# Optimization experiments

Hardware: AMD Instinct MI355X
Metric: run time of the kernel (lower is better)

Reference implementation:

```python
import jax, jax.numpy as jnp
import numpy as np

B, S, D = 1, 2048, 4096
H, KV = 32, 8
HD = D // H  # 128
NEG = -1e9


def _rope(t, cos, sin):
    # t: [B,S,h,HD]; cos/sin: [S,HD//2] -> broadcast [1,S,1,HD//2]
    tr = t[..., 0::2]
    ti = t[..., 1::2]
    c = cos[None, :, None, :]
    s = sin[None, :, None, :]
    out_r = tr * c - ti * s
    out_i = tr * s + ti * c
    # interleave back: (..., HD//2, 2) -> (..., HD)
    return jnp.stack([out_r, out_i], axis=-1).reshape(t.shape)


def setup_inputs() -> dict:
    key = jax.random.key(0)
    ks = jax.random.split(key, 5)
    w_scale = 0.02
    x = jax.random.normal(ks[0], (B, S, D), dtype=jnp.float32)
    wq = jax.random.normal(ks[1], (H * HD, D), dtype=jnp.float32) * w_scale
    wk = jax.random.normal(ks[2], (KV * HD, D), dtype=jnp.float32) * w_scale
    wv = jax.random.normal(ks[3], (KV * HD, D), dtype=jnp.float32) * w_scale
    wo = jax.random.normal(ks[4], (D, H * HD), dtype=jnp.float32) * w_scale
    # RoPE tables (theta = 10000)
    inv_freq = 1.0 / (10000.0 ** (np.arange(0, HD, 2, dtype=np.float32) / HD))
    angles = np.arange(S, dtype=np.float32)[:, None] * inv_freq[None, :]  # [S, HD//2]
    freqs_cos = jnp.asarray(np.cos(angles))
    freqs_sin = jnp.asarray(np.sin(angles))
    # causal additive mask [1,1,S,S]
    causal = jnp.tril(jnp.ones((S, S), dtype=bool))
    mask = jnp.where(causal, 0.0, NEG).astype(jnp.float32)[None, None]
    return {"x": x, "wq": wq, "wk": wk, "wv": wv, "wo": wo,
            "freqs_cos": freqs_cos, "freqs_sin": freqs_sin, "mask": mask}


def reference(x, wq, wk, wv, wo, freqs_cos, freqs_sin, mask):
    b, s, d = x.shape
    q = (x @ wq.T).reshape(b, s, H, HD)
    k = (x @ wk.T).reshape(b, s, KV, HD)
    v = (x @ wv.T).reshape(b, s, KV, HD)
    q = _rope(q, freqs_cos, freqs_sin)
    k = _rope(k, freqs_cos, freqs_sin)
    rep = H // KV
    k = jnp.repeat(k, rep, axis=2)  # [b,s,H,HD]
    v = jnp.repeat(v, rep, axis=2)
    scores = jnp.einsum('bshd,bthd->bhst', q, k) / jnp.sqrt(jnp.float32(HD))
    scores = scores + mask
    attn = jax.nn.softmax(scores, axis=-1)
    out = jnp.einsum('bhst,bthd->bshd', attn, v).reshape(b, s, H * HD)
    return out @ wo.T
```

## Files before the change

kernel.cpp:

```cpp
#include <hip/hip_runtime.h>
#include <hip/hip_bf16.h>
#include <math.h>

#define SEQ 2048
#define DIM 4096
#define NH 32
#define NKV 8
#define HD 128
#define KVD 1024
#define SCALE 0.08838834764831845f
#define NEGBIG -1000000000.0f

typedef __bf16 bf16;
typedef __attribute__((ext_vector_type(2))) __bf16 bf16x2;
typedef __attribute__((ext_vector_type(4))) __bf16 bf16x4;
typedef __attribute__((ext_vector_type(8))) __bf16 bf16x8;
typedef __attribute__((ext_vector_type(4))) float f32x4;

__device__ __forceinline__ void async_g2l16(const bf16* g, bf16* l) {
  __builtin_amdgcn_global_load_lds(
      (const __attribute__((address_space(1))) void*)g,
      (__attribute__((address_space(3))) void*)l,
      16, 0, 0);
}

#define SEG_X  2097152
#define SEG_WQ 4194304
#define SEG_WK 1048576
#define C0 SEG_X
#define C1 (C0 + SEG_WQ)
#define C2 (C1 + SEG_WK)
#define C3 (C2 + SEG_WK)
#define C4 (C3 + SEG_WQ)

__global__ void cast_all_kernel(const float* __restrict__ x,
                                const float* __restrict__ wq,
                                const float* __restrict__ wk,
                                const float* __restrict__ wv,
                                const float* __restrict__ wo,
                                bf16* __restrict__ xb, bf16* __restrict__ wqb,
                                bf16* __restrict__ wkb, bf16* __restrict__ wvb,
                                bf16* __restrict__ wob) {
  int i = blockIdx.x * 256 + threadIdx.x;
  const float* src; bf16* dst; int j;
  if (i < C0)      { src = x;  dst = xb;  j = i; }
  else if (i < C1) { src = wq; dst = wqb; j = i - C0; }
  else if (i < C2) { src = wk; dst = wkb; j = i - C1; }
  else if (i < C3) { src = wv; dst = wvb; j = i - C2; }
  else             { src = wo; dst = wob; j = i - C3; }
  float4 v = ((const float4*)src)[j];
  bf16x4 o;
  o[0] = (bf16)v.x; o[1] = (bf16)v.y; o[2] = (bf16)v.z; o[3] = (bf16)v.w;
  ((bf16x4*)dst)[j] = o;
}

__device__ __forceinline__ void gemm_core(
    const bf16* __restrict__ A, int lda,
    const bf16* __restrict__ B, int ldb,
    int K, int mBase, f32x4 acc[4][4])
{
  __shared__ __align__(16) bf16 As[128 * 32];
  __shared__ __align__(16) bf16 Bs[128 * 32];

  const int tid  = threadIdx.x;
  const int lane = tid & 63;
  const int w    = tid >> 6;
  const int l15  = lane & 15;
  const int quad = lane >> 4;
  const int wr   = (w >> 1) * 64;
  const int wc   = (w & 1) * 64;

  const int srow = lane >> 2;
  const int kswz = ((lane & 3) ^ ((srow >> 1) & 3)) * 8;
  const bf16* gA0 = A + (size_t)(mBase + w * 16 + srow) * lda + kswz;
  const bf16* gA1 = gA0 + (size_t)64 * lda;
  const bf16* gB0 = B + (size_t)(w * 16 + srow) * ldb + kswz;
  const bf16* gB1 = gB0 + (size_t)64 * ldb;
  bf16* lA0 = As + w * 512;
  bf16* lA1 = As + (w + 4) * 512;
  bf16* lB0 = Bs + w * 512;
  bf16* lB1 = Bs + (w + 4) * 512;

  const f32x4 vzero = {0.f, 0.f, 0.f, 0.f};
#pragma unroll
  for (int mi = 0; mi < 4; ++mi)
#pragma unroll
    for (int ni = 0; ni < 4; ++ni) acc[mi][ni] = vzero;

  const int rsw = ((l15 >> 1) & 3);

  for (int k0 = 0; k0 < K; k0 += 32) {
    __syncthreads();
    async_g2l16(gA0 + k0, lA0);
    async_g2l16(gA1 + k0, lA1);
    async_g2l16(gB0 + k0, lB0);
    async_g2l16(gB1 + k0, lB1);
    __syncthreads();

    bf16x8 a[4], b[4];
#pragma unroll
    for (int mi = 0; mi < 4; ++mi)
      a[mi] = *(const bf16x8*)(As + (wr + mi * 16 + l15) * 32 +
                               ((quad ^ rsw) * 8));
#pragma unroll
    for (int ni = 0; ni < 4; ++ni)
      b[ni] = *(const bf16x8*)(Bs + (wc + ni * 16 + l15) * 32 +
                               ((quad ^ rsw) * 8));
#pragma unroll
    for (int mi = 0; mi < 4; ++mi)
#pragma unroll
      for (int ni = 0; ni < 4; ++ni)
        acc[mi][ni] = __builtin_amdgcn_mfma_f32_16x16x32_bf16(
            a[mi], b[ni], acc[mi][ni], 0, 0, 0);
  }
}

__global__ __launch_bounds__(256, 2) void qkv_gemm_kernel(
    const bf16* __restrict__ xb, const bf16* __restrict__ wqb,
    const bf16* __restrict__ wkb, const bf16* __restrict__ wvb,
    const float* __restrict__ fc, const float* __restrict__ fs,
    bf16* __restrict__ Qb, bf16* __restrict__ Kb, bf16* __restrict__ Vt)
{
  const int nb = blockIdx.x;
  const int mBase = blockIdx.y * 128;
  const bf16* Bm;
  if (nb < 32)      Bm = wqb + (size_t)nb * 128 * DIM;
  else if (nb < 40) Bm = wkb + (size_t)(nb - 32) * 128 * DIM;
  else              Bm = wvb + (size_t)(nb - 40) * 128 * DIM;

  f32x4 acc[4][4];
  gemm_core(xb, DIM, Bm, DIM, DIM, mBase, acc);

  const int tid  = threadIdx.x;
  const int lane = tid & 63;
  const int w    = tid >> 6;
  const int l15  = lane & 15;
  const int quad = lane >> 4;
  const int wr   = (w >> 1) * 64;
  const int wc   = (w & 1) * 64;

  if (nb < 40) {
    const bool isQ = (nb < 32);
    bf16* dst = isQ ? (Qb + nb * HD) : (Kb + (nb - 32) * HD);
    const int ldd = isQ ? DIM : KVD;
    const float sc = isQ ? SCALE : 1.0f;
    const int odd = l15 & 1;
#pragma unroll
    for (int mi = 0; mi < 4; ++mi) {
#pragma unroll
      for (int ni = 0; ni < 4; ++ni) {
        int d = wc + ni * 16 + l15;
        int fidx = d >> 1;
#pragma unroll
        for (int r = 0; r < 4; ++r) {
          int s = mBase + wr + mi * 16 + quad * 4 + r;
          float v  = acc[mi][ni][r];
          float pv = __shfl_xor(v, 1, 64);
          float c  = fc[s * 64 + fidx];
          float sn = fs[s * 64 + fidx];
          float o  = odd ? (pv * sn + v * c) : (v * c - pv * sn);
          dst[(size_t)s * ldd + d] = (bf16)(o * sc);
        }
      }
    }
  } else {
    const int t = nb - 40;
#pragma unroll
    for (int mi = 0; mi < 4; ++mi) {
      int srow = mBase + wr + mi * 16 + quad * 4;
#pragma unroll
      for (int ni = 0; ni < 4; ++ni) {
        int d = wc + ni * 16 + l15;
        bf16x4 pv;
#pragma unroll
        for (int r = 0; r < 4; ++r) pv[r] = (bf16)acc[mi][ni][r];
        *(bf16x4*)(Vt + ((size_t)t * HD + d) * SEQ + srow) = pv;
      }
    }
  }
}

__global__ __launch_bounds__(256, 2) void out_gemm_kernel(
    const bf16* __restrict__ attnb, const bf16* __restrict__ wob,
    float* __restrict__ out)
{
  const int mBase = blockIdx.y * 128;
  f32x4 acc[4][4];
  gemm_core(attnb, DIM, wob + (size_t)blockIdx.x * 128 * DIM, DIM, DIM,
            mBase, acc);

  const int tid  = threadIdx.x;
  const int lane = tid & 63;
  const int w    = tid >> 6;
  const int l15  = lane & 15;
  const int quad = lane >> 4;
  const int wr   = (w >> 1) * 64;
  const int wc   = (w & 1) * 64;
#pragma unroll
  for (int mi = 0; mi < 4; ++mi) {
    int row = mBase + wr + mi * 16 + quad * 4;
#pragma unroll
    for (int ni = 0; ni < 4; ++ni) {
      int col = blockIdx.x * 128 + wc + ni * 16 + l15;
#pragma unroll
      for (int r = 0; r < 4; ++r)
        out[(size_t)(row + r) * DIM + col] = acc[mi][ni][r];
    }
  }
}

__global__ __launch_bounds__(256, 2) void attn_kernel(
    const bf16* __restrict__ Qb, const bf16* __restrict__ Kb,
    const bf16* __restrict__ Vt, bf16* __restrict__ attnb)
{
  __shared__ __align__(16) bf16 Ks[64 * 128];
  __shared__ __align__(16) bf16 Vs[128 * 64];
  __shared__ __align__(16) bf16 Ps[128 * 64];

  const int b    = blockIdx.x;
  const int half = b >> 8;
  const int r8   = b & 255;
  const int h    = (half << 4) | (r8 >> 4);
  const int qt   = half ? (r8 & 15) : 15 - (r8 & 15);
  const int kvh  = h >> 2;
  const int qbase = qt * 128;

  const int tid  = threadIdx.x;
  const int lane = tid & 63;
  const int w    = tid >> 6;
  const int l15  = lane & 15;
  const int quad = lane >> 4;

  bf16x8 qfrag[2][4];
#pragma unroll
  for (int n = 0; n < 2; ++n) {
    int q = qbase + w * 32 + n * 16 + l15;
#pragma unroll
    for (int ks = 0; ks < 4; ++ks)
      qfrag[n][ks] = *(const bf16x8*)(Qb + (size_t)q * DIM + h * HD +
                                      ks * 32 + quad * 8);
  }

  const f32x4 vzero = {0.f, 0.f, 0.f, 0.f};
  f32x4 oacc[8][2];
#pragma unroll
  for (int dm = 0; dm < 8; ++dm)
#pragma unroll
    for (int n = 0; n < 2; ++n) oacc[dm][n] = vzero;
  float m_run[2] = {-1e30f, -1e30f};
  float l_run[2] = {0.f, 0.f};

  const int nkt = 2 * (qt + 1);
  for (int kt = 0; kt < nkt; ++kt) {
    const int kbase = kt * 64;

    __syncthreads();
#pragma unroll
    for (int t = 0; t < 4; ++t) {
      int kr0 = w * 16 + t * 4;
      int krow = kr0 + (lane >> 4);
      int kg = (lane & 15) ^ (krow & 7);
      async_g2l16(Kb + (size_t)(kbase + krow) * KVD + kvh * HD + kg * 8,
                  Ks + kr0 * 128);
      int vr0 = w * 32 + t * 8;
      int d = vr0 + (lane >> 3);
      int vg = (lane & 7) ^ (d & 7);
      async_g2l16(Vt + ((size_t)kvh * HD + d) * SEQ + kbase + vg * 8,
                  Vs + vr0 * 64);
    }
    __syncthreads();

    f32x4 sacc[4][2];
#pragma unroll
    for (int kg = 0; kg < 4; ++kg)
#pragma unroll
      for (int n = 0; n < 2; ++n) sacc[kg][n] = vzero;
#pragma unroll
    for (int kg = 0; kg < 4; ++kg) {
      bf16x8 kf[4];
#pragma unroll
      for (int ks = 0; ks < 4; ++ks) {
        int row = kg * 16 + l15;
        kf[ks] = *(const bf16x8*)(Ks + row * 128 +
                                  (((ks * 4 + quad) ^ (row & 7)) * 8));
      }
#pragma unroll
      for (int n = 0; n < 2; ++n)
#pragma unroll
        for (int ks = 0; ks < 4; ++ks)
          sacc[kg][n] = __builtin_amdgcn_mfma_f32_16x16x32_bf16(
              kf[ks], qfrag[n][ks], sacc[kg][n], 0, 0, 0);
    }

#pragma unroll
    for (int n = 0; n < 2; ++n) {
      const int qloc = w * 32 + n * 16 + l15;
      const int qglob = qbase + qloc;
      if (kbase + 63 > qbase + w * 32 + n * 16) {
#pragma unroll
        for (int kg = 0; kg < 4; ++kg)
#pragma unroll
          for (int r = 0; r < 4; ++r) {
            int key = kbase + kg * 16 + quad * 4 + r;
            if (key > qglob) sacc[kg][n][r] = NEGBIG;
          }
      }
      float mx = -1e30f;
#pragma unroll
      for (int kg = 0; kg < 4; ++kg)
#pragma unroll
        for (int r = 0; r < 4; ++r) mx = fmaxf(mx, sacc[kg][n][r]);
      mx = fmaxf(mx, __shfl_xor(mx, 16, 64));
      mx = fmaxf(mx, __shfl_xor(mx, 32, 64));
      float mnew = fmaxf(m_run[n], mx);
      float alpha = __expf(m_run[n] - mnew);
      m_run[n] = mnew;
      float rs = 0.f;
#pragma unroll
      for (int kg = 0; kg < 4; ++kg) {
        bf16x4 pk;
#pragma unroll
        for (int r = 0; r < 4; ++r) {
          float p = __expf(sacc[kg][n][r] - mnew);
          rs += p;
          pk[r] = (bf16)p;
        }
        int g16 = (kg * 2 + (quad >> 1)) ^ (qloc & 7);
        *(bf16x4*)(Ps + qloc * 64 + g16 * 8 + (quad & 1) * 4) = pk;
      }
      rs += __shfl_xor(rs, 16, 64);
      rs += __shfl_xor(rs, 32, 64);
      l_run[n] = alpha * l_run[n] + rs;
#pragma unroll
      for (int dm = 0; dm < 8; ++dm)
#pragma unroll
        for (int r = 0; r < 4; ++r) oacc[dm][n][r] *= alpha;
    }

    bf16x8 pf[2][2];
#pragma unroll
    for (int kk = 0; kk < 2; ++kk)
#pragma unroll
      for (int n = 0; n < 2; ++n) {
        int qloc = w * 32 + n * 16 + l15;
        pf[kk][n] = *(const bf16x8*)(Ps + qloc * 64 +
                                     (((kk * 4 + quad) ^ (qloc & 7)) * 8));
      }
#pragma unroll
    for (int dm = 0; dm < 8; ++dm) {
#pragma unroll
      for (int kk = 0; kk < 2; ++kk) {
        int d = dm * 16 + l15;
        bf16x8 vf = *(const bf16x8*)(Vs + d * 64 +
                                     (((kk * 4 + quad) ^ (d & 7)) * 8));
#pragma unroll
        for (int n = 0; n < 2; ++n)
          oacc[dm][n] = __builtin_amdgcn_mfma_f32_16x16x32_bf16(
              vf, pf[kk][n], oacc[dm][n], 0, 0, 0);
      }
    }
  }

#pragma unroll
  for (int n = 0; n < 2; ++n) {
    float inv = 1.0f / l_run[n];
    int q = qbase + w * 32 + n * 16 + l15;
#pragma unroll
    for (int dm = 0; dm < 8; ++dm) {
      bf16x4 ov;
#pragma unroll
      for (int r = 0; r < 4; ++r) ov[r] = (bf16)(oacc[dm][n][r] * inv);
      *(bf16x4*)(attnb + (size_t)q * DIM + h * HD + dm * 16 + quad * 4) = ov;
    }
  }
}

extern "C" void kernel_launch(void* const* d_in, const int* in_sizes, int n_in,
                              void* d_out, int out_size, void* d_ws, size_t ws_size,
                              hipStream_t stream) {
  const float* x  = (const float*)d_in[0];
  const float* wq = (const float*)d_in[1];
  const float* wk = (const float*)d_in[2];
  const float* wv = (const float*)d_in[3];
  const float* wo = (const float*)d_in[4];
  const float* fc = (const float*)d_in[5];
  const float* fs = (const float*)d_in[6];
  float* out = (float*)d_out;

  size_t off = 0;
  char* wsb = (char*)d_ws;
  auto take = [&](size_t bytes) -> void* {
    void* p = wsb + off;
    off += (bytes + 255) & ~(size_t)255;
    return p;
  };
  bf16*  xb    = (bf16*)take((size_t)SEQ * DIM * 2);
  bf16*  wqb   = (bf16*)take((size_t)DIM * DIM * 2);
  bf16*  wkb   = (bf16*)take((size_t)KVD * DIM * 2);
  bf16*  wvb   = (bf16*)take((size_t)KVD * DIM * 2);
  bf16*  wob   = (bf16*)take((size_t)DIM * DIM * 2);
  bf16*  Qb    = (bf16*)take((size_t)SEQ * DIM * 2);
  bf16*  Kb    = (bf16*)take((size_t)SEQ * KVD * 2);
  bf16*  Vt    = (bf16*)take((size_t)NKV * HD * SEQ * 2);
  bf16*  attnb = (bf16*)take((size_t)SEQ * DIM * 2);

  cast_all_kernel<<<C4 / 256, 256, 0, stream>>>(x, wq, wk, wv, wo,
                                                xb, wqb, wkb, wvb, wob);

  qkv_gemm_kernel<<<dim3(48, 16), 256, 0, stream>>>(xb, wqb, wkb, wvb,
                                                    fc, fs, Qb, Kb, Vt);

  attn_kernel<<<dim3(512), 256, 0, stream>>>(Qb, Kb, Vt, attnb);

  out_gemm_kernel<<<dim3(32, 16), 256, 0, stream>>>(attnb, wob, out);
}
```

Measured before the change: 482.4 us.

## Replace GEMMs with 256x256 double-buffered, ping-pong scheduled 8-wave kernel

Both projection GEMMs now use a 256x256 block tile with 512 threads, K-tiles of 64, double-buffered LDS and async global-to-LDS loads interleaved between MFMA quarter-steps, with barriers and setprio to alternate waves between memory and math. This targets the old 128x128, K=32 single-buffer loop, which synchronised twice per step and exposed load latency. In exchange it uses a large LDS footprint (128KB) and high register pressure, and launches fewer blocks (192 and 128 across a 256-CU part), which may leave CUs idle.

Result: slower. 511.7 us (+6.1%).

```diff
diff --git a/kernel.cpp b/kernel.cpp
--- a/kernel.cpp
+++ b/kernel.cpp
@@ -12,7 +12,6 @@
 #define NEGBIG -1000000000.0f
 
 typedef __bf16 bf16;
-typedef __attribute__((ext_vector_type(2))) __bf16 bf16x2;
 typedef __attribute__((ext_vector_type(4))) __bf16 bf16x4;
 typedef __attribute__((ext_vector_type(8))) __bf16 bf16x8;
 typedef __attribute__((ext_vector_type(4))) float f32x4;
@@ -54,159 +53,235 @@
   ((bf16x4*)dst)[j] = o;
 }
 
-__device__ __forceinline__ void gemm_core(
-    const bf16* __restrict__ A, int lda,
-    const bf16* __restrict__ B, int ldb,
-    int K, int mBase, f32x4 acc[4][4])
+#define BAR()       asm volatile("s_barrier" ::: "memory")
+#define FENCE4()    asm volatile("s_waitcnt vmcnt(4)" ::: "memory")
+#define FENCE_ALL() asm volatile("s_waitcnt vmcnt(0)" ::: "memory")
+
+#define MFMAQ(AH, BC, MO, NO)                                              \
+  _Pragma("unroll") for (int m2 = 0; m2 < 4; ++m2)                         \
+  _Pragma("unroll") for (int n2 = 0; n2 < 2; ++n2)                         \
+  _Pragma("unroll") for (int kk = 0; kk < 2; ++kk)                         \
+    acc[(MO) + m2][(NO) + n2] = __builtin_amdgcn_mfma_f32_16x16x32_bf16(   \
+        (AH)[m2][kk], (BC)[n2][kk], acc[(MO) + m2][(NO) + n2], 0, 0, 0);
+
+__device__ __forceinline__ void gemm256_core(
+    const bf16* __restrict__ Ag,
+    const bf16* __restrict__ Bg,
+    f32x4 acc[8][4])
 {
-  __shared__ __align__(16) bf16 As[128 * 32];
-  __shared__ __align__(16) bf16 Bs[128 * 32];
+  __shared__ __align__(16) bf16 As[2 * 256 * 64];
+  __shared__ __align__(16) bf16 Bs[2 * 256 * 64];
 
   const int tid  = threadIdx.x;
   const int lane = tid & 63;
   const int w    = tid >> 6;
   const int l15  = lane & 15;
   const int quad = lane >> 4;
-  const int wr   = (w >> 1) * 64;
-  const int wc   = (w & 1) * 64;
-
-  const int srow = lane >> 2;
-  const int kswz = ((lane & 3) ^ ((srow >> 1) & 3)) * 8;
-  const bf16* gA0 = A + (size_t)(mBase + w * 16 + srow) * lda + kswz;
-  const bf16* gA1 = gA0 + (size_t)64 * lda;
-  const bf16* gB0 = B + (size_t)(w * 16 + srow) * ldb + kswz;
-  const bf16* gB1 = gB0 + (size_t)64 * ldb;
-  bf16* lA0 = As + w * 512;
-  bf16* lA1 = As + (w + 4) * 512;
-  bf16* lB0 = Bs + w * 512;
-  bf16* lB1 = Bs + (w + 4) * 512;
-
-  const f32x4 vzero = {0.f, 0.f, 0.f, 0.f};
-#pragma unroll
-  for (int mi = 0; mi < 4; ++mi)
-#pragma unroll
-    for (int ni = 0; ni < 4; ++ni) acc[mi][ni] = vzero;
-
-  const int rsw = ((l15 >> 1) & 3);
-
-  for (int k0 = 0; k0 < K; k0 += 32) {
-    __syncthreads();
-    async_g2l16(gA0 + k0, lA0);
-    async_g2l16(gA1 + k0, lA1);
-    async_g2l16(gB0 + k0, lB0);
-    async_g2l16(gB1 + k0, lB1);
-    __syncthreads();
-
-    bf16x8 a[4], b[4];
-#pragma unroll
-    for (int mi = 0; mi < 4; ++mi)
-      a[mi] = *(const bf16x8*)(As + (wr + mi * 16 + l15) * 32 +
-                               ((quad ^ rsw) * 8));
-#pragma unroll
-    for (int ni = 0; ni < 4; ++ni)
-      b[ni] = *(const bf16x8*)(Bs + (wc + ni * 16 + l15) * 32 +
-                               ((quad ^ rsw) * 8));
-#pragma unroll
-    for (int mi = 0; mi < 4; ++mi)
-#pragma unroll
-      for (int ni = 0; ni < 4; ++ni)
-        acc[mi][ni] = __builtin_amdgcn_mfma_f32_16x16x32_bf16(
-            a[mi], b[ni], acc[mi][ni], 0, 0, 0);
+  const int wr2  = (w >> 2) * 128;
+  const int wc2  = (w & 3) * 64;
+
+  const int srow = w * 8 + (lane >> 3);
+  const int sg8  = ((lane & 7) ^ (lane >> 3)) * 8;
+  const bf16* gA = Ag + (size_t)srow * DIM + sg8;
+  const bf16* gB = Bg + (size_t)srow * DIM + sg8;
+  bf16* lA = As + w * 512;
+  bf16* lB = Bs + w * 512;
+
+  const int g0   = (quad ^ (l15 & 7)) * 8;
+  const int g1   = g0 ^ 32;
+  const int aOff = (wr2 + l15) * 64;
+  const int bOff = (wc2 + l15) * 64;
+
+#define STAGE_A(b, kt)                                                     \
+  { _Pragma("unroll") for (int hh = 0; hh < 2; ++hh)                       \
+    _Pragma("unroll") for (int j = 0; j < 2; ++j)                          \
+      async_g2l16(gA + (size_t)(hh * 128 + j * 64) * DIM + (kt) * 64,      \
+                  lA + (b) * 16384 + (hh * 128 + j * 64) * 64); }
+#define STAGE_B0(b, kt)                                                    \
+  { _Pragma("unroll") for (int j = 0; j < 2; ++j)                          \
+      async_g2l16(gB + (size_t)(j * 64) * DIM + (kt) * 64,                 \
+                  lB + (b) * 16384 + (j * 64) * 64); }
+#define STAGE_B1(b, kt)                                                    \
+  { _Pragma("unroll") for (int j = 0; j < 2; ++j)                          \
+      async_g2l16(gB + (size_t)(128 + j * 64) * DIM + (kt) * 64,           \
+                  lB + (b) * 16384 + (128 + j * 64) * 64); }
+
+#define LDA(b, rh, m2, gk) \
+  (*(const bf16x8*)(As + (b) * 16384 + aOff + (rh) * 4096 + (m2) * 1024 + (gk)))
+#define LDB(b, ch, n2, gk) \
+  (*(const bf16x8*)(Bs + (b) * 16384 + bOff + (ch) * 2048 + (n2) * 1024 + (gk)))
+
+  const f32x4 vz = {0.f, 0.f, 0.f, 0.f};
+#pragma unroll
+  for (int mi = 0; mi < 8; ++mi)
+#pragma unroll
+    for (int ni = 0; ni < 4; ++ni) acc[mi][ni] = vz;
+
+  STAGE_A(0, 0); STAGE_B0(0, 0); STAGE_B1(0, 0);
+  STAGE_B0(1, 1); STAGE_B1(1, 1);
+  FENCE4();
+  BAR();
+
+  for (int i = 0; i < 32; ++i) {
+    const int ktn0 = (2 * i + 2 > 63) ? 63 : 2 * i + 2;
+    const int ktn1 = (2 * i + 3 > 63) ? 63 : 2 * i + 3;
+    {
+      bf16x8 aH[4][2], bC0[2][2], bC1[2][2];
+#pragma unroll
+      for (int m2 = 0; m2 < 4; ++m2) { aH[m2][0] = LDA(0, 0, m2, g0); aH[m2][1] = LDA(0, 0, m2, g1); }
+#pragma unroll
+      for (int n2 = 0; n2 < 2; ++n2) { bC0[n2][0] = LDB(0, 0, n2, g0); bC0[n2][1] = LDB(0, 0, n2, g1); }
+      STAGE_A(1, 2 * i + 1);
+      BAR(); __builtin_amdgcn_s_setprio(1);
+      MFMAQ(aH, bC0, 0, 0);
+      __builtin_amdgcn_s_setprio(0); BAR();
+#pragma unroll
+      for (int n2 = 0; n2 < 2; ++n2) { bC1[n2][0] = LDB(0, 1, n2, g0); bC1[n2][1] = LDB(0, 1, n2, g1); }
+      BAR(); __builtin_amdgcn_s_setprio(1);
+      MFMAQ(aH, bC1, 0, 2);
+      __builtin_amdgcn_s_setprio(0); BAR();
+#pragma unroll
+      for (int m2 = 0; m2 < 4; ++m2) { aH[m2][0] = LDA(0, 1, m2, g0); aH[m2][1] = LDA(0, 1, m2, g1); }
+      STAGE_B0(0, ktn0);
+      BAR(); __builtin_amdgcn_s_setprio(1);
+      MFMAQ(aH, bC1, 4, 2);
+      __builtin_amdgcn_s_setprio(0); BAR();
+      STAGE_B1(0, ktn0);
+      FENCE4();
+      BAR(); __builtin_amdgcn_s_setprio(1);
+      MFMAQ(aH, bC0, 4, 0);
+      __builtin_amdgcn_s_setprio(0); BAR();
+    }
+    {
+      bf16x8 aH[4][2], bC0[2][2], bC1[2][2];
+#pragma unroll
+      for (int m2 = 0; m2 < 4; ++m2) { aH[m2][0] = LDA(1, 0, m2, g0); aH[m2][1] = LDA(1, 0, m2, g1); }
+#pragma unroll
+      for (int n2 = 0; n2 < 2; ++n2) { bC0[n2][0] = LDB(1, 0, n2, g0); bC0[n2][1] = LDB(1, 0, n2, g1); }
+      STAGE_A(0, ktn0);
+      BAR(); __builtin_amdgcn_s_setprio(1);
+      MFMAQ(aH, bC0, 0, 0);
+      __builtin_amdgcn_s_setprio(0); BAR();
+#pragma unroll
+      for (int n2 = 0; n2 < 2; ++n2) { bC1[n2][0] = LDB(1, 1, n2, g0); bC1[n2][1] = LDB(1, 1, n2, g1); }
+      BAR(); __builtin_amdgcn_s_setprio(1);
+      MFMAQ(aH, bC1, 0, 2);
+      __builtin_amdgcn_s_setprio(0); BAR();
+#pragma unroll
+      for (int m2 = 0; m2 < 4; ++m2) { aH[m2][0] = LDA(1, 1, m2, g0); aH[m2][1] = LDA(1, 1, m2, g1); }
+      STAGE_B0(1, ktn1);
+      BAR(); __builtin_amdgcn_s_setprio(1);
+      MFMAQ(aH, bC1, 4, 2);
+      __builtin_amdgcn_s_setprio(0); BAR();
+      STAGE_B1(1, ktn1);
+      FENCE4();
+      BAR(); __builtin_amdgcn_s_setprio(1);
+      MFMAQ(aH, bC0, 4, 0);
+      __builtin_amdgcn_s_setprio(0); BAR();
+    }
   }
-}
-
-__global__ __launch_bounds__(256, 2) void qkv_gemm_kernel(
+  FENCE_ALL();
+}
+
+__global__ __launch_bounds__(512, 2) void qkv256_kernel(
     const bf16* __restrict__ xb, const bf16* __restrict__ wqb,
     const bf16* __restrict__ wkb, const bf16* __restrict__ wvb,
     const float* __restrict__ fc, const float* __restrict__ fs,
     bf16* __restrict__ Qb, bf16* __restrict__ Kb, bf16* __restrict__ Vt)
 {
-  const int nb = blockIdx.x;
-  const int mBase = blockIdx.y * 128;
-  const bf16* Bm;
-  if (nb < 32)      Bm = wqb + (size_t)nb * 128 * DIM;
-  else if (nb < 40) Bm = wkb + (size_t)(nb - 32) * 128 * DIM;
-  else              Bm = wvb + (size_t)(nb - 40) * 128 * DIM;
-
-  f32x4 acc[4][4];
-  gemm_core(xb, DIM, Bm, DIM, DIM, mBase, acc);
+  const int bid   = blockIdx.x;
+  const int mTile = bid & 7;
+  const int nTile = bid >> 3;
+  const bf16* Bg;
+  if (nTile < 16)      Bg = wqb + (size_t)nTile * 256 * DIM;
+  else if (nTile < 20) Bg = wkb + (size_t)(nTile - 16) * 256 * DIM;
+  else                 Bg = wvb + (size_t)(nTile - 20) * 256 * DIM;
+
+  f32x4 acc[8][4];
+  gemm256_core(xb + (size_t)mTile * 256 * DIM, Bg, acc);
 
   const int tid  = threadIdx.x;
   const int lane = tid & 63;
   const int w    = tid >> 6;
   const int l15  = lane & 15;
   const int quad = lane >> 4;
-  const int wr   = (w >> 1) * 64;
-  const int wc   = (w & 1) * 64;
-
-  if (nb < 40) {
-    const bool isQ = (nb < 32);
-    bf16* dst = isQ ? (Qb + nb * HD) : (Kb + (nb - 32) * HD);
-    const int ldd = isQ ? DIM : KVD;
+  const int wr2  = (w >> 2) * 128;
+  const int wc2  = (w & 3) * 64;
+  const int sBase = mTile * 256 + wr2 + quad * 4;
+  const int nBase = nTile * 256 + wc2;
+
+  if (nTile < 20) {
+    const bool isQ = nTile < 16;
+    bf16* dst      = isQ ? Qb : Kb;
+    const int ldd  = isQ ? DIM : KVD;
     const float sc = isQ ? SCALE : 1.0f;
-    const int odd = l15 & 1;
-#pragma unroll
-    for (int mi = 0; mi < 4; ++mi) {
+    const int cOff = isQ ? nBase : nBase - 4096;
+    const int odd  = l15 & 1;
+#pragma unroll
+    for (int mi = 0; mi < 8; ++mi)
 #pragma unroll
       for (int ni = 0; ni < 4; ++ni) {
-        int d = wc + ni * 16 + l15;
-        int fidx = d >> 1;
+        const int n    = nBase + ni * 16 + l15;
+        const int fidx = (n >> 1) & 63;
+        const int col  = cOff + ni * 16 + l15;
 #pragma unroll
         for (int r = 0; r < 4; ++r) {
-          int s = mBase + wr + mi * 16 + quad * 4 + r;
+          const int s = sBase + mi * 16 + r;
           float v  = acc[mi][ni][r];
           float pv = __shfl_xor(v, 1, 64);
           float c  = fc[s * 64 + fidx];
           float sn = fs[s * 64 + fidx];
           float o  = odd ? (pv * sn + v * c) : (v * c - pv * sn);
-          dst[(size_t)s * ldd + d] = (bf16)(o * sc);
+          dst[(size_t)s * ldd + col] = (bf16)(o * sc);
         }
       }
-    }
   } else {
-    const int t = nb - 40;
-#pragma unroll
-    for (int mi = 0; mi < 4; ++mi) {
-      int srow = mBase + wr + mi * 16 + quad * 4;
+    const int vBase = nBase - 5120;
+#pragma unroll
+    for (int mi = 0; mi < 8; ++mi) {
+      const int sb = sBase + mi * 16;
 #pragma unroll
       for (int ni = 0; ni < 4; ++ni) {
-        int d = wc + ni * 16 + l15;
+        const int nv = vBase + ni * 16 + l15;
+        const int t = nv >> 7, d = nv & 127;
         bf16x4 pv;
 #pragma unroll
         for (int r = 0; r < 4; ++r) pv[r] = (bf16)acc[mi][ni][r];
-        *(bf16x4*)(Vt + ((size_t)t * HD + d) * SEQ + srow) = pv;
+        *(bf16x4*)(Vt + ((size_t)t * HD + d) * SEQ + sb) = pv;
       }
     }
   }
 }
 
-__global__ __launch_bounds__(256, 2) void out_gemm_kernel(
+__global__ __launch_bounds__(512, 2) void out256_kernel(
     const bf16* __restrict__ attnb, const bf16* __restrict__ wob,
     float* __restrict__ out)
 {
-  const int mBase = blockIdx.y * 128;
-  f32x4 acc[4][4];
-  gemm_core(attnb, DIM, wob + (size_t)blockIdx.x * 128 * DIM, DIM, DIM,
-            mBase, acc);
+  const int bid   = blockIdx.x;
+  const int mTile = bid & 7;
+  const int nTile = bid >> 3;
+
+  f32x4 acc[8][4];
+  gemm256_core(attnb + (size_t)mTile * 256 * DIM,
+               wob + (size_t)nTile * 256 * DIM, acc);
 
   const int tid  = threadIdx.x;
   const int lane = tid & 63;
   const int w    = tid >> 6;
   const int l15  = lane & 15;
   const int quad = lane >> 4;
-  const int wr   = (w >> 1) * 64;
-  const int wc   = (w & 1) * 64;
-#pragma unroll
-  for (int mi = 0; mi < 4; ++mi) {
-    int row = mBase + wr + mi * 16 + quad * 4;
+  const int wr2  = (w >> 2) * 128;
+  const int wc2  = (w & 3) * 64;
+  const int sBase = mTile * 256 + wr2 + quad * 4;
+#pragma unroll
+  for (int mi = 0; mi < 8; ++mi)
 #pragma unroll
     for (int ni = 0; ni < 4; ++ni) {
-      int col = blockIdx.x * 128 + wc + ni * 16 + l15;
+      const int col = nTile * 256 + wc2 + ni * 16 + l15;
 #pragma unroll
       for (int r = 0; r < 4; ++r)
-        out[(size_t)(row + r) * DIM + col] = acc[mi][ni][r];
-    }
-  }
+        out[(size_t)(sBase + mi * 16 + r) * DIM + col] = acc[mi][ni][r];
+    }
 }
 
 __global__ __launch_bounds__(256, 2) void attn_kernel(
@@ -407,10 +482,10 @@
   cast_all_kernel<<<C4 / 256, 256, 0, stream>>>(x, wq, wk, wv, wo,
                                                 xb, wqb, wkb, wvb, wob);
 
-  qkv_gemm_kernel<<<dim3(48, 16), 256, 0, stream>>>(xb, wqb, wkb, wvb,
-                                                    fc, fs, Qb, Kb, Vt);
+  qkv256_kernel<<<dim3(192), 512, 0, stream>>>(xb, wqb, wkb, wvb,
+                                               fc, fs, Qb, Kb, Vt);
 
   attn_kernel<<<dim3(512), 256, 0, stream>>>(Qb, Kb, Vt, attnb);
 
-  out_gemm_kernel<<<dim3(32, 16), 256, 0, stream>>>(attnb, wob, out);
-}
+  out256_kernel<<<dim3(128), 512, 0, stream>>>(attnb, wob, out);
+}
```
